# Optimization experiments

Hardware: AMD Instinct MI355X
Metric: run time of the kernel (lower is better)

The kernel has to match this reference:

```python
import jax, jax.numpy as jnp
import numpy as np

NUM_HEADS = 16
EMB_DIM = 1024
IN_CH = 512
D_CTX = 768
DEPTH = EMB_DIM // NUM_HEADS
SCALE = DEPTH ** -0.5
NEG = -1e9


def setup_inputs() -> dict:
    key = jax.random.key(0)
    ks = jax.random.split(key, 12)
    B, N, S = 4, 4096, 256
    def lin(kw, fan_in, fan_out):
        lim = 1.0 / np.sqrt(fan_in)
        w = jax.random.uniform(kw, (fan_out, fan_in), jnp.float32, -lim, lim)
        return w
    return {
        'x': jax.random.normal(ks[0], (B, N, IN_CH), jnp.float32),
        'context': jax.random.normal(ks[1], (B, S, D_CTX), jnp.float32),
        'pad_mask': jnp.ones((B, N), jnp.float32),
        'seq_mask': jnp.ones((B, S), jnp.float32),
        'Wq_w': lin(ks[2], IN_CH, EMB_DIM), 'Wq_b': jnp.zeros((EMB_DIM,), jnp.float32),
        'Wk_w': lin(ks[3], D_CTX, EMB_DIM), 'Wk_b': jnp.zeros((EMB_DIM,), jnp.float32),
        'Wv_w': lin(ks[4], D_CTX, EMB_DIM), 'Wv_b': jnp.zeros((EMB_DIM,), jnp.float32),
        'P1_w': lin(ks[5], EMB_DIM, EMB_DIM), 'P1_b': jnp.zeros((EMB_DIM,), jnp.float32),
        'P2_w': lin(ks[6], EMB_DIM, IN_CH), 'P2_b': jnp.zeros((IN_CH,), jnp.float32),
    }


def reference(x, context, pad_mask, seq_mask, Wq_w, Wq_b, Wk_w, Wk_b, Wv_w, Wv_b, P1_w, P1_b, P2_w, P2_b):
    B, N, _ = x.shape
    S = context.shape[1]
    # QKV projections, split into heads: [B, H, N|S, D]
    Q = (x @ Wq_w.T + Wq_b).reshape(B, N, NUM_HEADS, DEPTH).transpose(0, 2, 1, 3)
    K = (context @ Wk_w.T + Wk_b).reshape(B, S, NUM_HEADS, DEPTH).transpose(0, 2, 1, 3)
    V = (context @ Wv_w.T + Wv_b).reshape(B, S, NUM_HEADS, DEPTH).transpose(0, 2, 1, 3)
    # attention scores [B, H, N, S]
    att = jnp.einsum('bnid,bnjd->bnij', Q, K) * SCALE
    # outer-product mask: pad_mask[B,N] x seq_mask[B,S] -> [B,1,N,S]
    mask = (pad_mask[:, :, None] * seq_mask[:, None, :])[:, None, :, :]
    att = jnp.where(mask != 0.0, att, NEG)
    att = jax.nn.softmax(att, axis=-1)
    out = jnp.einsum('bnij,bnjd->bnid', att, V)
    out = out.transpose(0, 2, 1, 3).reshape(B, N, EMB_DIM)
    # proj_out MLP: Linear -> ReLU -> Linear
    out = jax.nn.relu(out @ P1_w.T + P1_b) @ P2_w.T + P2_b
    return out
```

## Files before the change

### kernel.cpp

```cpp
#include <hip/hip_runtime.h>
#include <hip/hip_bf16.h>
#include <stdint.h>

typedef __attribute__((ext_vector_type(8))) short bf16x8;
typedef __attribute__((ext_vector_type(4))) short s16x4;
typedef __attribute__((ext_vector_type(4))) float f32x4;

#define MFMA16(a, b, c) __builtin_amdgcn_mfma_f32_16x16x32_bf16((a), (b), (c), 0, 0, 0)
#define MFMAH(a, b, c) __builtin_amdgcn_mfma_f32_16x16x16bf16_1k((a), (b), (c), 0, 0, 0)

__device__ __forceinline__ void gload_lds16(const void* g, void* l) {
  __builtin_amdgcn_global_load_lds((const __attribute__((address_space(1))) void*)g,
                                   (__attribute__((address_space(3))) void*)l, 16, 0, 0);
}

__global__ void cvt_all(const float* __restrict__ s0, const float* __restrict__ s1,
                        const float* __restrict__ s2, const float* __restrict__ s3,
                        const float* __restrict__ s4, const float* __restrict__ s5,
                        const float* __restrict__ s6,
                        __hip_bfloat16* __restrict__ d0, __hip_bfloat16* __restrict__ d1,
                        __hip_bfloat16* __restrict__ d2, __hip_bfloat16* __restrict__ d3,
                        __hip_bfloat16* __restrict__ d4, __hip_bfloat16* __restrict__ d5,
                        __hip_bfloat16* __restrict__ d6) {
  constexpr int e0 = 2097152;
  constexpr int e1 = e0 + 196608;
  constexpr int e2 = e1 + 131072;
  constexpr int e3 = e2 + 196608;
  constexpr int e4 = e3 + 196608;
  constexpr int e5 = e4 + 262144;
  constexpr int e6 = e5 + 131072;
  const int stride = gridDim.x * blockDim.x;
  for (int i = blockIdx.x * blockDim.x + threadIdx.x; i < e6; i += stride) {
    const float* s; __hip_bfloat16* d; int j;
    if (i < e0)      { s = s0; d = d0; j = i; }
    else if (i < e1) { s = s1; d = d1; j = i - e0; }
    else if (i < e2) { s = s2; d = d2; j = i - e1; }
    else if (i < e3) { s = s3; d = d3; j = i - e2; }
    else if (i < e4) { s = s4; d = d4; j = i - e3; }
    else if (i < e5) { s = s5; d = d5; j = i - e4; }
    else             { s = s6; d = d6; j = i - e5; }
    const float4 v = *(const float4*)(s + (size_t)j * 4);
    s16x4 o;
    __hip_bfloat16 h;
    h = __float2bfloat16(v.x); o[0] = *(short*)&h;
    h = __float2bfloat16(v.y); o[1] = *(short*)&h;
    h = __float2bfloat16(v.z); o[2] = *(short*)&h;
    h = __float2bfloat16(v.w); o[3] = *(short*)&h;
    *(s16x4*)((short*)d + (size_t)j * 4) = o;
  }
}


template <int RELU, int OUTMODE>
__global__ __launch_bounds__(256, 2) void gemm_bt(
    const __hip_bfloat16* __restrict__ Abf, const __hip_bfloat16* __restrict__ Wbf,
    const float* __restrict__ bias, void* __restrict__ Cv,
    int M, int N, int K) {
  __shared__ __align__(16) __hip_bfloat16 As[128 * 32];
  __shared__ __align__(16) __hip_bfloat16 Bs[128 * 32];
  const int t = threadIdx.x;
  const int w = t >> 6, lane = t & 63;
  const int lr = lane & 15, lg = lane >> 4;
  const int m0 = blockIdx.x * 128, n0 = blockIdx.y * 128;
  const int wr = (w >> 1) * 64, wc = (w & 1) * 64;

  const char* Ag = (const char*)Abf;
  const char* Wg = (const char*)Wbf;
  const size_t ldb = (size_t)K * 2;

  f32x4 acc[4][4] = {};

  const int o0 = (w << 10) + lane * 16;
  const int o1 = o0 + 4096;
  const int r0 = o0 >> 6, gc0 = ((((o0 >> 4) & 3) ^ ((r0 >> 1) & 3)) << 4);
  const int r1 = o1 >> 6, gc1 = ((((o1 >> 4) & 3) ^ ((r1 >> 1) & 3)) << 4);
  const int slx = (lg ^ ((lr >> 1) & 3)) << 4;

  for (int kt = 0; kt < K; kt += 32) {
    if (kt) __syncthreads();
    gload_lds16(Ag + (size_t)(m0 + r0) * ldb + kt * 2 + gc0, (char*)As + (w << 10));
    gload_lds16(Ag + (size_t)(m0 + r1) * ldb + kt * 2 + gc1, (char*)As + 4096 + (w << 10));
    gload_lds16(Wg + (size_t)(n0 + r0) * ldb + kt * 2 + gc0, (char*)Bs + (w << 10));
    gload_lds16(Wg + (size_t)(n0 + r1) * ldb + kt * 2 + gc1, (char*)Bs + 4096 + (w << 10));
    __syncthreads();

    bf16x8 af[4], bfv[4];
#pragma unroll
    for (int mi = 0; mi < 4; ++mi)
      af[mi] = *(const bf16x8*)((const char*)As + ((wr + mi * 16 + lr) << 6) + slx);
#pragma unroll
    for (int ni = 0; ni < 4; ++ni)
      bfv[ni] = *(const bf16x8*)((const char*)Bs + ((wc + ni * 16 + lr) << 6) + slx);
#pragma unroll
    for (int mi = 0; mi < 4; ++mi)
#pragma unroll
      for (int ni = 0; ni < 4; ++ni)
        acc[mi][ni] = MFMA16(af[mi], bfv[ni], acc[mi][ni]);
  }

#pragma unroll
  for (int ni = 0; ni < 4; ++ni) {
    const int col = n0 + wc + ni * 16 + lr;
    const float bv = bias[col];
#pragma unroll
    for (int mi = 0; mi < 4; ++mi) {
      const int row = m0 + wr + mi * 16 + lg * 4;
#pragma unroll
      for (int j = 0; j < 4; ++j) {
        float v = acc[mi][ni][j] + bv;
        if (RELU) v = fmaxf(v, 0.0f);
        if (OUTMODE == 0) {
          ((__hip_bfloat16*)Cv)[(size_t)(row + j) * N + col] = __float2bfloat16(v);
        } else if (OUTMODE == 1) {
          ((float*)Cv)[(size_t)(row + j) * N + col] = v;
        } else {
          const int rb = (row + j) >> 8, s = (row + j) & 255;
          const int hh = col >> 6, d = col & 63;
          ((__hip_bfloat16*)Cv)[(((size_t)(rb * 16 + hh) * 64 + d) << 8) + s] =
              __float2bfloat16(v);
        }
      }
    }
  }
}

__device__ __forceinline__ void gemm256_body(
    const __hip_bfloat16* __restrict__ Abf, const __hip_bfloat16* __restrict__ Wbf,
    const float* __restrict__ bias, __hip_bfloat16* __restrict__ C,
    int N, int K, int outmode, int relu, int bx, int by) {
  __shared__ __align__(16) __hip_bfloat16 AsB[4][256 * 32];
  __shared__ __align__(16) __hip_bfloat16 BsB[4][256 * 32];
  const int t = threadIdx.x;
  const int w = t >> 6, lane = t & 63;
  const int lr = lane & 15, lg = lane >> 4;
  const int m0 = bx * 256, n0 = by * 256;
  const int wr = (w >> 2) * 128, wc = (w & 3) * 64;

  const char* Ag = (const char*)Abf;
  const char* Wg = (const char*)Wbf;
  const size_t ldb = (size_t)K * 2;

  f32x4 acc[8][4] = {};

  const int o0 = (w << 10) + lane * 16;
  const int o1 = o0 + 8192;
  const int r0 = o0 >> 6, gc0 = ((((o0 >> 4) & 3) ^ ((r0 >> 1) & 3)) << 4);
  const int r1 = o1 >> 6, gc1 = ((((o1 >> 4) & 3) ^ ((r1 >> 1) & 3)) << 4);
  const int slx = (lg ^ ((lr >> 1) & 3)) << 4;
  const int db0 = (w << 10);
  const int db1 = 8192 + (w << 10);

  auto STAGE = [&](int buf, int tile) {
    const int kt = tile << 5;
    gload_lds16(Ag + (size_t)(m0 + r0) * ldb + kt * 2 + gc0, (char*)AsB[buf] + db0);
    gload_lds16(Ag + (size_t)(m0 + r1) * ldb + kt * 2 + gc1, (char*)AsB[buf] + db1);
    gload_lds16(Wg + (size_t)(n0 + r0) * ldb + kt * 2 + gc0, (char*)BsB[buf] + db0);
    gload_lds16(Wg + (size_t)(n0 + r1) * ldb + kt * 2 + gc1, (char*)BsB[buf] + db1);
  };
  auto COMPUTE = [&](int buf) {
    bf16x8 af[8], bfv[4];
#pragma unroll
    for (int mi = 0; mi < 8; ++mi)
      af[mi] = *(const bf16x8*)((const char*)AsB[buf] + ((wr + mi * 16 + lr) << 6) + slx);
#pragma unroll
    for (int ni = 0; ni < 4; ++ni)
      bfv[ni] = *(const bf16x8*)((const char*)BsB[buf] + ((wc + ni * 16 + lr) << 6) + slx);
#pragma unroll
    for (int mi = 0; mi < 8; ++mi)
#pragma unroll
      for (int ni = 0; ni < 4; ++ni)
        acc[mi][ni] = MFMA16(af[mi], bfv[ni], acc[mi][ni]);
  };

  const int nt = K >> 5;
  STAGE(0, 0);
  STAGE(1, 1);
  STAGE(2, 2);
  for (int j = 0; j < nt - 3; ++j) {
    STAGE((j + 3) & 3, j + 3);
    asm volatile("s_waitcnt vmcnt(12)" ::: "memory");
    __builtin_amdgcn_s_barrier();
    COMPUTE(j & 3);
    __builtin_amdgcn_s_barrier();
  }
  asm volatile("s_waitcnt vmcnt(8)" ::: "memory");
  __builtin_amdgcn_s_barrier();
  COMPUTE((nt - 3) & 3);
  __builtin_amdgcn_s_barrier();
  asm volatile("s_waitcnt vmcnt(4)" ::: "memory");
  __builtin_amdgcn_s_barrier();
  COMPUTE((nt - 2) & 3);
  __builtin_amdgcn_s_barrier();
  asm volatile("s_waitcnt vmcnt(0)" ::: "memory");
  __builtin_amdgcn_s_barrier();
  COMPUTE((nt - 1) & 3);

#pragma unroll
  for (int ni = 0; ni < 4; ++ni) {
    const int col = n0 + wc + ni * 16 + lr;
    const float bv = bias[col];
#pragma unroll
    for (int mi = 0; mi < 8; ++mi) {
      const int row = m0 + wr + mi * 16 + lg * 4;
#pragma unroll
      for (int j = 0; j < 4; ++j) {
        float v = acc[mi][ni][j] + bv;
        if (relu) v = fmaxf(v, 0.0f);
        if (outmode == 0) {
          C[(size_t)(row + j) * N + col] = __float2bfloat16(v);
        } else {
          const int rb = (row + j) >> 8, s = (row + j) & 255;
          const int hh = col >> 6, d = col & 63;
          C[(((size_t)(rb * 16 + hh) * 64 + d) << 8) + s] = __float2bfloat16(v);
        }
      }
    }
  }
}

__global__ __launch_bounds__(512, 2) void gemm256_qkv(
    const __hip_bfloat16* __restrict__ xb, const __hip_bfloat16* __restrict__ ctxb,
    const __hip_bfloat16* __restrict__ Wq, const __hip_bfloat16* __restrict__ Wk,
    const __hip_bfloat16* __restrict__ Wv,
    const float* __restrict__ bq, const float* __restrict__ bk, const float* __restrict__ bv,
    __hip_bfloat16* __restrict__ Q, __hip_bfloat16* __restrict__ Kp,
    __hip_bfloat16* __restrict__ Vt) {
  const int bid = blockIdx.x;
  if (bid < 16) {
    gemm256_body(ctxb, Wk, bk, Kp, 1024, 768, 0, 0, bid >> 2, bid & 3);
  } else if (bid < 32) {
    const int l = bid - 16;
    gemm256_body(ctxb, Wv, bv, Vt, 1024, 768, 2, 0, l >> 2, l & 3);
  } else {
    const int l = bid - 32;
    gemm256_body(xb, Wq, bq, Q, 1024, 512, 0, 0, l >> 2, l & 3);
  }
}

__global__ __launch_bounds__(512, 2) void gemm256_p1(
    const __hip_bfloat16* __restrict__ A, const __hip_bfloat16* __restrict__ W,
    const float* __restrict__ bias, __hip_bfloat16* __restrict__ C) {
  const int bid = blockIdx.x;
  gemm256_body(A, W, bias, C, 1024, 1024, 0, 1, bid >> 2, bid & 3);
}

__global__ __launch_bounds__(512, 4) void attn_fused(
    const __hip_bfloat16* __restrict__ Qb, const __hip_bfloat16* __restrict__ Kb,
    const __hip_bfloat16* __restrict__ Vtg, const float* __restrict__ padm,
    const float* __restrict__ seqm, __hip_bfloat16* __restrict__ O) {
  constexpr int S = 256, E = 1024, Nq = 4096;
  constexpr float NEGV = -1e9f;
  __shared__ __align__(16) char smem[65536];
  char* VtB = smem;
  char* KsB = smem + 32768;

  const int t = threadIdx.x;
  const int w = t >> 6, lane = t & 63;
  const int lr = lane & 15, lg = lane >> 4;
  const int h = blockIdx.y, b = blockIdx.z;

  const char* Kg = (const char*)(Kb + (size_t)b * S * E + h * 64);
#pragma unroll
  for (int i = 0; i < 4; ++i) {
    const int o = ((i * 8 + w) << 10) + lane * 16;
    const int s = o >> 7, bc = o & 127;
    gload_lds16(Kg + (size_t)s * (E * 2) + (bc ^ ((s & 7) << 4)), KsB + ((i * 8 + w) << 10));
  }
  const char* Vg = (const char*)Vtg + ((size_t)(b * 16 + h) << 15);
#pragma unroll
  for (int i = 0; i < 4; ++i) {
    const int o = ((i * 8 + w) << 10) + lane * 16;
    const int d = o >> 9, c = o & 511;
    gload_lds16(Vg + (d << 9) + (c ^ ((d & 7) << 4)), VtB + ((i * 8 + w) << 10));
  }

  const int qw = blockIdx.x * 128 + w * 16;
  const short* Qg = (const short*)Qb + (size_t)(b * Nq + qw + lr) * E + h * 64;
  const bf16x8 aq0 = *(const bf16x8*)(Qg + (lg << 3));
  const bf16x8 aq1 = *(const bf16x8*)(Qg + 32 + (lg << 3));
  const float padq = padm[(size_t)b * Nq + qw + lr];
  const float qbias = (padq != 0.f) ? 0.f : NEGV;

  __syncthreads();

  const int swz = (lr & 7) << 4;
  f32x4 o[4] = {};
  float ssum = 0.f;
#pragma unroll
  for (int ni = 0; ni < 16; ++ni) {
    const int s = ni * 16 + lr;
    const bf16x8 bk0 = *(const bf16x8*)(KsB + (s << 7) + ((lg << 4) ^ swz));
    const bf16x8 bk1 = *(const bf16x8*)(KsB + (s << 7) + ((64 + (lg << 4)) ^ swz));
    f32x4 a = {};
    a = MFMA16(bk0, aq0, a);
    a = MFMA16(bk1, aq1, a);

    const float4 sm4 = *(const float4*)(seqm + (size_t)b * S + ni * 16 + lg * 4);
    const float e0 = __expf(a[0] * 0.125f + ((sm4.x != 0.f ? 0.f : NEGV) + qbias));
    const float e1 = __expf(a[1] * 0.125f + ((sm4.y != 0.f ? 0.f : NEGV) + qbias));
    const float e2 = __expf(a[2] * 0.125f + ((sm4.z != 0.f ? 0.f : NEGV) + qbias));
    const float e3 = __expf(a[3] * 0.125f + ((sm4.w != 0.f ? 0.f : NEGV) + qbias));
    ssum += (e0 + e1) + (e2 + e3);

    s16x4 pf;
    __hip_bfloat16 hh;
    hh = __float2bfloat16(e0); pf[0] = *(short*)&hh;
    hh = __float2bfloat16(e1); pf[1] = *(short*)&hh;
    hh = __float2bfloat16(e2); pf[2] = *(short*)&hh;
    hh = __float2bfloat16(e3); pf[3] = *(short*)&hh;

    const int sb = (ni * 32 + lg * 8);
#pragma unroll
    for (int nd = 0; nd < 4; ++nd) {
      const int d = nd * 16 + lr;
      const s16x4 bv = *(const s16x4*)(VtB + (d << 9) + (sb ^ swz));
      o[nd] = MFMAH(pf, bv, o[nd]);
    }
  }

  ssum += __shfl_xor(ssum, 16);
  ssum += __shfl_xor(ssum, 32);
  const float inv = 1.0f / ssum;
  float invj[4];
#pragma unroll
  for (int j = 0; j < 4; ++j) invj[j] = __shfl(inv, lg * 4 + j);

  __hip_bfloat16* Og = O + (size_t)(b * Nq + qw) * E + h * 64;
#pragma unroll
  for (int nd = 0; nd < 4; ++nd)
#pragma unroll
    for (int j = 0; j < 4; ++j)
      Og[(size_t)(lg * 4 + j) * E + nd * 16 + lr] = __float2bfloat16(o[nd][j] * invj[j]);
}

extern "C" void kernel_launch(void* const* d_in, const int* in_sizes, int n_in,
                              void* d_out, int out_size, void* d_ws, size_t ws_size,
                              hipStream_t stream) {
  const float* x    = (const float*)d_in[0];
  const float* ctx  = (const float*)d_in[1];
  const float* padm = (const float*)d_in[2];
  const float* seqm = (const float*)d_in[3];
  const float* Wq_w = (const float*)d_in[4];
  const float* Wq_b = (const float*)d_in[5];
  const float* Wk_w = (const float*)d_in[6];
  const float* Wk_b = (const float*)d_in[7];
  const float* Wv_w = (const float*)d_in[8];
  const float* Wv_b = (const float*)d_in[9];
  const float* P1_w = (const float*)d_in[10];
  const float* P1_b = (const float*)d_in[11];
  const float* P2_w = (const float*)d_in[12];
  const float* P2_b = (const float*)d_in[13];
  float* out = (float*)d_out;

  char* ws = (char*)d_ws;
  size_t off = 0;
  auto alloc = [&](size_t bytes) { char* p = ws + off; off += (bytes + 255) & ~(size_t)255; return p; };
  __hip_bfloat16* Q    = (__hip_bfloat16*)alloc(16384ull * 1024 * 2);
  __hip_bfloat16* AO   = (__hip_bfloat16*)alloc(16384ull * 1024 * 2);
  __hip_bfloat16* xb   = (__hip_bfloat16*)alloc(16384ull * 512 * 2);
  __hip_bfloat16* ctxb = (__hip_bfloat16*)alloc(1024ull * 768 * 2);
  __hip_bfloat16* Kp   = (__hip_bfloat16*)alloc(1024ull * 1024 * 2);
  __hip_bfloat16* Vt   = (__hip_bfloat16*)alloc(1024ull * 1024 * 2);
  __hip_bfloat16* Wqb  = (__hip_bfloat16*)alloc(1024ull * 512 * 2);
  __hip_bfloat16* Wkb  = (__hip_bfloat16*)alloc(1024ull * 768 * 2);
  __hip_bfloat16* Wvb  = (__hip_bfloat16*)alloc(1024ull * 768 * 2);
  __hip_bfloat16* P1b  = (__hip_bfloat16*)alloc(1024ull * 1024 * 2);
  __hip_bfloat16* P2b  = (__hip_bfloat16*)alloc(512ull * 1024 * 2);
  __hip_bfloat16* O1   = Q;

  cvt_all<<<dim3(2048, 1, 1), dim3(256, 1, 1), 0, stream>>>(
      x, ctx, Wq_w, Wk_w, Wv_w, P1_w, P2_w, xb, ctxb, Wqb, Wkb, Wvb, P1b, P2b);

  gemm256_qkv<<<dim3(288, 1, 1), dim3(512, 1, 1), 0, stream>>>(
      xb, ctxb, Wqb, Wkb, Wvb, Wq_b, Wk_b, Wv_b, Q, Kp, Vt);
  attn_fused<<<dim3(32, 16, 4), dim3(512, 1, 1), 0, stream>>>(Q, Kp, Vt, padm, seqm, AO);
  gemm256_p1<<<dim3(256, 1, 1), dim3(512, 1, 1), 0, stream>>>(AO, P1b, P1_b, O1);
  gemm_bt<0, 1><<<dim3(128, 4, 1), dim3(256, 1, 1), 0, stream>>>(O1, P2b, P2_b, out, 16384, 512, 1024);
}
```

Before: 172.3 us.

## Split GEMM k-tile into two interleaved halves with priority and XCD-aware block remap

Restructures the 256x256 bf16 GEMM main loop so each k-tile is computed in two halves (rows 0-63 and 64-127 of the warp tile). The A and B global-to-LDS loads for the stage three tiles ahead are issued between the halves, with explicit barriers, lgkmcnt waits and s_setprio around the MFMA blocks to overlap memory traffic with math. It also remaps block indices in the Q projection and P1 GEMMs so that consecutive blocks land on different XCDs, aiming to improve L2 locality. The added barriers per tile and the hand-tuned waitcnts could add synchronization overhead.

```diff
diff --git a/kernel.cpp b/kernel.cpp
--- a/kernel.cpp
+++ b/kernel.cpp
@@ -150,50 +150,70 @@
   const int db0 = (w << 10);
   const int db1 = 8192 + (w << 10);
 
-  auto STAGE = [&](int buf, int tile) {
+  auto STAGE_A = [&](int buf, int tile) {
     const int kt = tile << 5;
     gload_lds16(Ag + (size_t)(m0 + r0) * ldb + kt * 2 + gc0, (char*)AsB[buf] + db0);
     gload_lds16(Ag + (size_t)(m0 + r1) * ldb + kt * 2 + gc1, (char*)AsB[buf] + db1);
+  };
+  auto STAGE_B = [&](int buf, int tile) {
+    const int kt = tile << 5;
     gload_lds16(Wg + (size_t)(n0 + r0) * ldb + kt * 2 + gc0, (char*)BsB[buf] + db0);
     gload_lds16(Wg + (size_t)(n0 + r1) * ldb + kt * 2 + gc1, (char*)BsB[buf] + db1);
   };
-  auto COMPUTE = [&](int buf) {
-    bf16x8 af[8], bfv[4];
-#pragma unroll
-    for (int mi = 0; mi < 8; ++mi)
-      af[mi] = *(const bf16x8*)((const char*)AsB[buf] + ((wr + mi * 16 + lr) << 6) + slx);
+
+  auto tile_body = [&](int j, int stage_tile, int vmsel) {
+    const int buf = j & 3;
+    const int nbuf = stage_tile & 3;
+    bf16x8 af0[4], af1[4], bfv[4];
+#pragma unroll
+    for (int mi = 0; mi < 4; ++mi)
+      af0[mi] = *(const bf16x8*)((const char*)AsB[buf] + ((wr + mi * 16 + lr) << 6) + slx);
 #pragma unroll
     for (int ni = 0; ni < 4; ++ni)
       bfv[ni] = *(const bf16x8*)((const char*)BsB[buf] + ((wc + ni * 16 + lr) << 6) + slx);
-#pragma unroll
-    for (int mi = 0; mi < 8; ++mi)
+    if (stage_tile >= 0) STAGE_A(nbuf, stage_tile);
+    asm volatile("s_barrier" ::: "memory");
+    asm volatile("s_waitcnt lgkmcnt(0)" ::: "memory");
+    __builtin_amdgcn_sched_barrier(0);
+    __builtin_amdgcn_s_setprio(1);
+#pragma unroll
+    for (int mi = 0; mi < 4; ++mi)
 #pragma unroll
       for (int ni = 0; ni < 4; ++ni)
-        acc[mi][ni] = MFMA16(af[mi], bfv[ni], acc[mi][ni]);
+        acc[mi][ni] = MFMA16(af0[mi], bfv[ni], acc[mi][ni]);
+    __builtin_amdgcn_s_setprio(0);
+    asm volatile("s_barrier" ::: "memory");
+#pragma unroll
+    for (int mi = 0; mi < 4; ++mi)
+      af1[mi] = *(const bf16x8*)((const char*)AsB[buf] + ((wr + (mi + 4) * 16 + lr) << 6) + slx);
+    if (stage_tile >= 0) STAGE_B(nbuf, stage_tile);
+    if (vmsel == 0)      asm volatile("s_waitcnt vmcnt(8)" ::: "memory");
+    else if (vmsel == 1) asm volatile("s_waitcnt vmcnt(4)" ::: "memory");
+    else if (vmsel == 2) asm volatile("s_waitcnt vmcnt(0)" ::: "memory");
+    asm volatile("s_barrier" ::: "memory");
+    asm volatile("s_waitcnt lgkmcnt(0)" ::: "memory");
+    __builtin_amdgcn_sched_barrier(0);
+    __builtin_amdgcn_s_setprio(1);
+#pragma unroll
+    for (int mi = 0; mi < 4; ++mi)
+#pragma unroll
+      for (int ni = 0; ni < 4; ++ni)
+        acc[mi + 4][ni] = MFMA16(af1[mi], bfv[ni], acc[mi + 4][ni]);
+    __builtin_amdgcn_s_setprio(0);
+    asm volatile("s_barrier" ::: "memory");
   };
 
   const int nt = K >> 5;
-  STAGE(0, 0);
-  STAGE(1, 1);
-  STAGE(2, 2);
-  for (int j = 0; j < nt - 3; ++j) {
-    STAGE((j + 3) & 3, j + 3);
-    asm volatile("s_waitcnt vmcnt(12)" ::: "memory");
-    __builtin_amdgcn_s_barrier();
-    COMPUTE(j & 3);
-    __builtin_amdgcn_s_barrier();
-  }
+  STAGE_A(0, 0); STAGE_B(0, 0);
+  STAGE_A(1, 1); STAGE_B(1, 1);
+  STAGE_A(2, 2); STAGE_B(2, 2);
   asm volatile("s_waitcnt vmcnt(8)" ::: "memory");
-  __builtin_amdgcn_s_barrier();
-  COMPUTE((nt - 3) & 3);
-  __builtin_amdgcn_s_barrier();
-  asm volatile("s_waitcnt vmcnt(4)" ::: "memory");
-  __builtin_amdgcn_s_barrier();
-  COMPUTE((nt - 2) & 3);
-  __builtin_amdgcn_s_barrier();
-  asm volatile("s_waitcnt vmcnt(0)" ::: "memory");
-  __builtin_amdgcn_s_barrier();
-  COMPUTE((nt - 1) & 3);
+  asm volatile("s_barrier" ::: "memory");
+  for (int j = 0; j < nt - 3; ++j)
+    tile_body(j, j + 3, 0);
+  tile_body(nt - 3, -1, 1);
+  tile_body(nt - 2, -1, 2);
+  tile_body(nt - 1, -1, 3);
 
 #pragma unroll
   for (int ni = 0; ni < 4; ++ni) {
@@ -233,7 +253,8 @@
     gemm256_body(ctxb, Wv, bv, Vt, 1024, 768, 2, 0, l >> 2, l & 3);
   } else {
     const int l = bid - 32;
-    gemm256_body(xb, Wq, bq, Q, 1024, 512, 0, 0, l >> 2, l & 3);
+    const int rb = (l & 7) * 32 + (l >> 3);
+    gemm256_body(xb, Wq, bq, Q, 1024, 512, 0, 0, rb >> 2, rb & 3);
   }
 }
 
@@ -241,7 +262,8 @@
     const __hip_bfloat16* __restrict__ A, const __hip_bfloat16* __restrict__ W,
     const float* __restrict__ bias, __hip_bfloat16* __restrict__ C) {
   const int bid = blockIdx.x;
-  gemm256_body(A, W, bias, C, 1024, 1024, 0, 1, bid >> 2, bid & 3);
+  const int rb = (bid & 7) * 32 + (bid >> 3);
+  gemm256_body(A, W, bias, C, 1024, 1024, 0, 1, rb >> 2, rb & 3);
 }
 
 __global__ __launch_bounds__(512, 4) void attn_fused(
```

After: 169.8 us. About the same (-1.5%).
